# Kernel tuning notes

Hardware: AMD Instinct MI355X
Metric: run time of the kernel (lower is better)

Reference implementation:

```python
import jax, jax.numpy as jnp
import numpy as np

B, T, C, HEAD = 8, 4096, 64, 64

def setup_inputs() -> dict:
    key = jax.random.key(0)
    kx, kk, kq, kv = jax.random.split(key, 4)
    x = jax.random.normal(kx, (B, T, C), dtype=jnp.float32)
    # nn.Linear(n_embd, head_size, bias=False) weight has shape (head_size, n_embd)
    s = 1.0 / np.sqrt(C)
    Wk = jax.random.uniform(kk, (HEAD, C), dtype=jnp.float32, minval=-s, maxval=s)
    Wq = jax.random.uniform(kq, (HEAD, C), dtype=jnp.float32, minval=-s, maxval=s)
    Wv = jax.random.uniform(kv, (HEAD, C), dtype=jnp.float32, minval=-s, maxval=s)
    return {"x": x, "Wk": Wk, "Wq": Wq, "Wv": Wv}

def reference(x, Wk, Wq, Wv):
    Bq, Tq, Cq = x.shape
    k = jnp.einsum('btc,hc->bth', x, Wk)   # (B,T,head)
    q = jnp.einsum('btc,hc->bth', x, Wq)
    v = jnp.einsum('btc,hc->bth', x, Wv)
    scale = Cq ** (-0.5)                    # note: scales by input dim C, as in source
    wei = jnp.einsum('bth,bsh->bts', q, k) * scale  # (B,T,T)
    causal = jnp.tril(jnp.ones((Tq, Tq), dtype=bool))
    wei = jnp.where(causal, wei, -jnp.inf)
    wei = jax.nn.softmax(wei, axis=-1)      # dropout p=0.0 -> no-op
    out = jnp.einsum('bts,bsh->bth', wei, v)
    return out
```

## Files before the change

kernel.cpp:

```cpp
#include <hip/hip_runtime.h>
#include <hip/hip_bf16.h>
#include <math.h>

#define BB 8
#define TT 4096
#define HD 64

typedef __attribute__((ext_vector_type(8))) short short8;
typedef __attribute__((ext_vector_type(4))) float f32x4;
typedef __attribute__((ext_vector_type(16))) float f32x16;
typedef __attribute__((ext_vector_type(2))) unsigned int uint2v;
typedef __attribute__((ext_vector_type(4))) unsigned int uint4v;

#define LOG2E 1.44269504088896f

__device__ __forceinline__ unsigned pack_bf2(float a, float b) {
    unsigned r;
    asm("v_cvt_pk_bf16_f32 %0, %1, %2" : "=v"(r) : "v"(a), "v"(b));
    return r;
}
__device__ __forceinline__ unsigned short bfbits(float f) {
    unsigned r;
    asm("v_cvt_pk_bf16_f32 %0, %1, %2" : "=v"(r) : "v"(f), "v"(f));
    return (unsigned short)r;
}
__device__ __forceinline__ float bf2f(unsigned short u) {
    unsigned v = (unsigned)u << 16;
    return __builtin_bit_cast(float, v);
}
__device__ __forceinline__ float fexp2(float x) {
    return __builtin_amdgcn_exp2f(x);
}
__device__ __forceinline__ short8 cvt8(float4 a, float4 b, float sc) {
    uint4v u;
    u[0] = pack_bf2(a.x * sc, a.y * sc);
    u[1] = pack_bf2(a.z * sc, a.w * sc);
    u[2] = pack_bf2(b.x * sc, b.y * sc);
    u[3] = pack_bf2(b.z * sc, b.w * sc);
    return __builtin_bit_cast(short8, u);
}

__global__ __launch_bounds__(256) void qkv_proj_mfma(
    const float* __restrict__ x,
    const float* __restrict__ Wk, const float* __restrict__ Wq, const float* __restrict__ Wv,
    unsigned short* __restrict__ qo, unsigned short* __restrict__ ko,
    unsigned short* __restrict__ vto)
{
    __shared__ short lds[20480];
    short* xls = lds;
    short* wls = lds + 8192;

    const int tid = threadIdx.x;
    const int l = tid & 63, w = tid >> 6;
    const int hi = l >> 5, c31 = l & 31;
    const long t0 = (long)blockIdx.x * 128;
    const int b = (int)(t0 >> 12);
    const int tl0 = (int)(t0 & 4095);

#pragma unroll
    for (int i = 0; i < 4; ++i) {
        int slot = tid + 256 * i;
        int row = slot >> 3, bl = slot & 7;
        const float* xp = x + (t0 + row) * 64 + 8 * bl;
        float4 a = *(const float4*)xp;
        float4 bq = *(const float4*)(xp + 4);
        *(short8*)&xls[row * 64 + 8 * (bl ^ (row & 7))] = cvt8(a, bq, 1.f);
    }
#pragma unroll
    for (int i = 0; i < 6; ++i) {
        int slot = tid + 256 * i;
        int row = slot >> 3, bl = slot & 7;
        const float* wp;
        float sc;
        if (row < 64)       { wp = Wq + row * 64;         sc = 0.125f * LOG2E; }
        else if (row < 128) { wp = Wk + (row - 64) * 64;  sc = 1.f; }
        else                { wp = Wv + (row - 128) * 64; sc = 1.f; }
        wp += 8 * bl;
        float4 a = *(const float4*)wp;
        float4 bq = *(const float4*)(wp + 4);
        *(short8*)&wls[row * 64 + 8 * (bl ^ (row & 7))] = cvt8(a, bq, sc);
    }
    __syncthreads();

    short8 xf[4];
#pragma unroll
    for (int ki = 0; ki < 4; ++ki) {
        int row = 32 * w + c31;
        xf[ki] = *(const short8*)&xls[row * 64 + 8 * ((2 * ki + hi) ^ (row & 7))];
    }
    f32x16 cqk[4] = {};
#pragma unroll
    for (int nt = 0; nt < 4; ++nt) {
#pragma unroll
        for (int ki = 0; ki < 4; ++ki) {
            int row = 32 * nt + c31;
            short8 wf = *(const short8*)&wls[row * 64 + 8 * ((2 * ki + hi) ^ (row & 7))];
            cqk[nt] = __builtin_amdgcn_mfma_f32_32x32x16_bf16(xf[ki], wf, cqk[nt], 0, 0, 0);
        }
    }
    f32x16 cv[2] = {};
#pragma unroll
    for (int rt = 0; rt < 2; ++rt) {
#pragma unroll
        for (int ki = 0; ki < 4; ++ki) {
            int row = 128 + 32 * rt + c31;
            short8 wf = *(const short8*)&wls[row * 64 + 8 * ((2 * ki + hi) ^ (row & 7))];
            cv[rt] = __builtin_amdgcn_mfma_f32_32x32x16_bf16(wf, xf[ki], cv[rt], 0, 0, 0);
        }
    }
#pragma unroll
    for (int rt = 0; rt < 2; ++rt) {
#pragma unroll
        for (int r = 0; r < 16; ++r) {
            int h = 32 * rt + (r & 3) + 8 * (r >> 2) + 4 * hi;
            vto[((long)b * 64 + h) * 4096 + tl0 + 32 * w + c31] = bfbits(cv[rt][r]);
        }
    }

    __syncthreads();
    short* cb = lds;
#pragma unroll
    for (int nt = 0; nt < 4; ++nt) {
#pragma unroll
        for (int r = 0; r < 16; ++r) {
            int trow = 32 * w + (r & 3) + 8 * (r >> 2) + 4 * hi;
            cb[trow * 136 + 32 * nt + c31] = (short)bfbits(cqk[nt][r]);
        }
    }
    __syncthreads();
    {
        int row = tid >> 1, seg = tid & 1;
        const short8* cp = (const short8*)&cb[row * 136 + seg * 64];
        unsigned short* dst = (seg == 0 ? qo : ko) + (t0 + row) * 64;
#pragma unroll
        for (int i = 0; i < 8; ++i) ((short8*)dst)[i] = cp[i];
    }
}

__global__ __launch_bounds__(256, 3) void attn_mfma(
    const unsigned short* __restrict__ qg,
    const unsigned short* __restrict__ kg,
    const unsigned short* __restrict__ vtg,
    unsigned short* __restrict__ Opart,
    float2* __restrict__ ml,
    float* __restrict__ outg)
{
    __shared__ short kls[3][4096];
    __shared__ short vls[3][4096];

    const int tid = threadIdx.x;
    const int l = tid & 63, w = tid >> 6;
    const int q = l & 31, hi = l >> 5;
    const int qs7 = q & 7;

    const int bid = blockIdx.x;
    const int b = bid & 7;
    const int j = bid >> 3;
    int qt = 0, ci = 0;
    {
        int acc = 0;
        for (int qq = 31; qq >= 0; --qq) {
            int nc = (2 * qq + 17) >> 4;
            if (j < acc + nc) { qt = qq; ci = j - acc; break; }
            acc += nc;
        }
    }
    const int nch = (2 * qt + 17) >> 4;
    int ntile = 2 * qt + 2 - 16 * ci;
    if (ntile > 16) ntile = 16;
    const int c0 = ci * 1024;

    const int q0w = qt * 128 + 32 * w;
    const int qr = q0w + q;
    const int lastg = (q0w + 31) >> 6;

    const unsigned short* qb = qg + ((long)b * TT + qr) * HD;
    short8 qf[4];
#pragma unroll
    for (int ki = 0; ki < 4; ++ki) qf[ki] = *(const short8*)(qb + 16 * ki + 8 * hi);

    int ofs[2][4];
#pragma unroll
    for (int a = 0; a < 2; ++a)
#pragma unroll
        for (int i2 = 0; i2 < 4; ++i2)
            ofs[a][i2] = (32 * a + q) * 128 + 16 * ((2 * i2 + hi) ^ qs7);

    f32x16 oacc[2] = {};
    float m = -INFINITY, lsum = 0.f;

    const unsigned short* kbase = kg + (long)b * TT * HD;
    const unsigned short* vbase = vtg + (long)b * HD * TT;

    const int r8 = l >> 3;
    const int blsw = (l & 7) ^ r8;
    const long koff0 = (long)(8 * w + r8) * HD + 8 * blsw;
    const long voff0 = (long)(8 * w + r8) * TT + 8 * blsw;

#define STAGE(buf_, s_) do {                                                            \
    _Pragma("unroll")                                                                   \
    for (int c_ = 0; c_ < 2; ++c_) {                                                    \
        const unsigned short* kp_ = kbase + (long)(s_) * HD + koff0 + (long)c_ * 32 * HD; \
        const unsigned short* vp_ = vbase + (s_) + voff0 + (long)c_ * 32 * TT;          \
        short* kd_ = &kls[buf_][2048 * c_ + 512 * w];                                   \
        short* vd_ = &vls[buf_][2048 * c_ + 512 * w];                                   \
        __builtin_amdgcn_global_load_lds((const __attribute__((address_space(1))) void*)kp_, \
                                         (__attribute__((address_space(3))) void*)kd_, 16, 0, 0); \
        __builtin_amdgcn_global_load_lds((const __attribute__((address_space(1))) void*)vp_, \
                                         (__attribute__((address_space(3))) void*)vd_, 16, 0, 0); \
    }                                                                                   \
} while (0)

    STAGE(0, c0);
    if (ntile > 1) STAGE(1, c0 + 64);

    int cur = 0, nxt2 = 2;
    for (int it = 0; it < ntile; ++it) {
        const int s0 = c0 + (it << 6);
        if (it + 1 < ntile) asm volatile("s_waitcnt vmcnt(4)" ::: "memory");
        else                asm volatile("s_waitcnt vmcnt(0)" ::: "memory");
        __builtin_amdgcn_s_barrier();
        __builtin_amdgcn_sched_barrier(0);
        if (it + 2 < ntile) STAGE(nxt2, s0 + 128);

        if (s0 <= q0w + 31) {
            const int gti = ci * 16 + it;
            const int nkt = (gti == lastg && (w & 1) == 0) ? 1 : 2;
            const short* kb_ = kls[cur];
            const short* vb_ = vls[cur];

            f32x16 sacc[2] = {};
            __builtin_amdgcn_s_setprio(1);
#pragma unroll
            for (int kt = 0; kt < 2; ++kt) {
                if (kt < nkt) {
#pragma unroll
                    for (int ki = 0; ki < 4; ++ki) {
                        short8 kf = *(const short8*)((const char*)kb_ + ofs[kt][ki]);
                        sacc[kt] = __builtin_amdgcn_mfma_f32_32x32x16_bf16(kf, qf[ki], sacc[kt], 0, 0, 0);
                    }
                }
            }
            __builtin_amdgcn_s_setprio(0);

            if (gti == lastg) {
#pragma unroll
                for (int kt = 0; kt < 2; ++kt) {
                    if (kt >= nkt) continue;
#pragma unroll
                    for (int r = 0; r < 16; ++r) {
                        int kkg = s0 + 32 * kt + (r & 3) + 8 * (r >> 2) + 4 * hi;
                        if (kkg > qr) sacc[kt][r] = -INFINITY;
                    }
                }
            }

            float t8[8];
#pragma unroll
            for (int r = 0; r < 8; ++r) {
                float a = fmaxf(sacc[0][r], sacc[0][r + 8]);
                if (nkt == 2) a = fmaxf(a, fmaxf(sacc[1][r], sacc[1][r + 8]));
                t8[r] = a;
            }
            float pmax = fmaxf(fmaxf(fmaxf(t8[0], t8[1]), fmaxf(t8[2], t8[3])),
                               fmaxf(fmaxf(t8[4], t8[5]), fmaxf(t8[6], t8[7])));
            if (__any(pmax > m + 11.0f)) {
                pmax = fmaxf(pmax, __shfl_xor(pmax, 32, 64));
                float mn = fmaxf(m, pmax);
                float fac = fexp2(m - mn);
                lsum *= fac;
                oacc[0] *= fac;
                oacc[1] *= fac;
                m = mn;
            }

            float rsum = 0.f;
            unsigned ulo[8], uhi[8];
#pragma unroll
            for (int kt = 0; kt < 2; ++kt) {
#pragma unroll
                for (int jj = 0; jj < 4; ++jj) {
                    if (kt < nkt) {
                        float p0 = fexp2(sacc[kt][4 * jj + 0] - m);
                        float p1 = fexp2(sacc[kt][4 * jj + 1] - m);
                        float p2 = fexp2(sacc[kt][4 * jj + 2] - m);
                        float p3 = fexp2(sacc[kt][4 * jj + 3] - m);
                        rsum += (p0 + p1) + (p2 + p3);
                        ulo[4 * kt + jj] = pack_bf2(p0, p1);
                        uhi[4 * kt + jj] = pack_bf2(p2, p3);
                    } else {
                        ulo[4 * kt + jj] = 0;
                        uhi[4 * kt + jj] = 0;
                    }
                }
            }
            lsum += rsum;

            const int nks = 2 * nkt;
#pragma unroll
            for (int ks = 0; ks < 4; ++ks) {
                if (ks >= nks) continue;
                uint2v rlo = __builtin_amdgcn_permlane32_swap(ulo[2 * ks], ulo[2 * ks + 1], false, false);
                uint2v rhi = __builtin_amdgcn_permlane32_swap(uhi[2 * ks], uhi[2 * ks + 1], false, false);
                uint4v paw;
                paw[0] = rlo[0]; paw[1] = rhi[0]; paw[2] = rlo[1]; paw[3] = rhi[1];
                short8 pa = __builtin_bit_cast(short8, paw);
                __builtin_amdgcn_s_setprio(1);
#pragma unroll
                for (int dt = 0; dt < 2; ++dt) {
                    short8 vf = *(const short8*)((const char*)vb_ + ofs[dt][ks]);
                    oacc[dt] = __builtin_amdgcn_mfma_f32_32x32x16_bf16(vf, pa, oacc[dt], 0, 0, 0);
                }
                __builtin_amdgcn_s_setprio(0);
            }
        }
        cur = (cur == 2) ? 0 : cur + 1;
        nxt2 = (nxt2 == 2) ? 0 : nxt2 + 1;
    }
#undef STAGE

    lsum += __shfl_xor(lsum, 32, 64);

    const int lr = 32 * w + q;
    if (nch == 1) {
        const float inv = 1.f / lsum;
        float* op = outg + ((long)b * TT + qr) * HD;
#pragma unroll
        for (int dt = 0; dt < 2; ++dt) {
#pragma unroll
            for (int jj = 0; jj < 4; ++jj) {
                f32x4 o4;
                o4[0] = oacc[dt][4 * jj + 0] * inv;
                o4[1] = oacc[dt][4 * jj + 1] * inv;
                o4[2] = oacc[dt][4 * jj + 2] * inv;
                o4[3] = oacc[dt][4 * jj + 3] * inv;
                *(f32x4*)(op + 32 * dt + 8 * jj + 4 * hi) = o4;
            }
        }
    } else {
        const float inv = lsum > 0.f ? 1.f / lsum : 0.f;
        unsigned short* po = Opart + ((long)(b * 80 + j) * 128 + lr) * 64;
#pragma unroll
        for (int dt = 0; dt < 2; ++dt) {
#pragma unroll
            for (int jj = 0; jj < 4; ++jj) {
                uint2v u;
                u[0] = pack_bf2(oacc[dt][4 * jj + 0] * inv, oacc[dt][4 * jj + 1] * inv);
                u[1] = pack_bf2(oacc[dt][4 * jj + 2] * inv, oacc[dt][4 * jj + 3] * inv);
                *(uint2v*)(po + 32 * dt + 8 * jj + 4 * hi) = u;
            }
        }
        ml[(long)(b * 80 + j) * 128 + lr] = make_float2(m, lsum);
    }
}

__global__ __launch_bounds__(256) void combine(
    const unsigned short* __restrict__ Opart,
    const float2* __restrict__ ml,
    float* __restrict__ outg)
{
    const int bid = blockIdx.x;
    const int b = bid & 7, qt = 8 + (bid >> 3);
    const int nc = (2 * qt + 17) >> 4;
    int jb = 0;
    for (int qq = 31; qq > qt; --qq) jb += (2 * qq + 17) >> 4;

    const int tid = threadIdx.x;
    const int row = tid >> 1, dh = (tid & 1) * 32;
    const long base = (long)(b * 80 + jb) * 128 + row;

    float mv[4], lv[4], M = -INFINITY;
#pragma unroll
    for (int c = 0; c < 4; ++c) {
        mv[c] = -INFINITY; lv[c] = 0.f;
        if (c < nc) {
            float2 t = ml[base + (long)c * 128];
            mv[c] = t.x; lv[c] = t.y;
            M = fmaxf(M, mv[c]);
        }
    }
    float L = 0.f, wt[4];
#pragma unroll
    for (int c = 0; c < 4; ++c) {
        wt[c] = (c < nc) ? lv[c] * fexp2(mv[c] - M) : 0.f;
        L += wt[c];
    }
    float acc[32];
#pragma unroll
    for (int i = 0; i < 32; ++i) acc[i] = 0.f;
#pragma unroll
    for (int c = 0; c < 4; ++c) {
        if (c < nc && wt[c] > 0.f) {
            const short8* op = (const short8*)(Opart + (base + (long)c * 128) * 64 + dh);
#pragma unroll
            for (int i = 0; i < 4; ++i) {
                short8 v = op[i];
#pragma unroll
                for (int e = 0; e < 8; ++e)
                    acc[8 * i + e] += wt[c] * bf2f((unsigned short)v[e]);
            }
        }
    }
    const float invL = 1.f / L;
    float* dst = outg + ((long)b * TT + qt * 128 + row) * HD + dh;
#pragma unroll
    for (int i = 0; i < 8; ++i) {
        f32x4 o;
        o[0] = acc[4 * i + 0] * invL; o[1] = acc[4 * i + 1] * invL;
        o[2] = acc[4 * i + 2] * invL; o[3] = acc[4 * i + 3] * invL;
        *(f32x4*)(dst + 4 * i) = o;
    }
}

extern "C" void kernel_launch(void* const* d_in, const int* in_sizes, int n_in,
                              void* d_out, int out_size, void* d_ws, size_t ws_size,
                              hipStream_t stream) {
    const float* x  = (const float*)d_in[0];
    const float* Wk = (const float*)d_in[1];
    const float* Wq = (const float*)d_in[2];
    const float* Wv = (const float*)d_in[3];
    float* out = (float*)d_out;

    const long N = (long)BB * TT * HD;
    unsigned short* q16 = (unsigned short*)d_ws;
    unsigned short* k16 = q16 + N;
    unsigned short* vt16 = k16 + N;
    unsigned short* Opart = (unsigned short*)((char*)d_ws + 12 * 1024 * 1024);
    float2* mlp = (float2*)((char*)d_ws + 23068672);

    qkv_proj_mfma<<<BB * TT / 128, 256, 0, stream>>>(x, Wk, Wq, Wv, q16, k16, vt16);
    attn_mfma<<<8 * 80, 256, 0, stream>>>(q16, k16, vt16, Opart, mlp, out);
    combine<<<8 * 24, 256, 0, stream>>>(Opart, mlp, out);
}
```

Measured before the change: 61.98 us.

## Give each attention wave two 32-row query tiles to reuse K/V LDS fragments

Each attention block now runs 2 waves instead of 4, and each wave handles 64 query rows as two 32-row tiles (A and B). The K and V fragments read from LDS are shared across both tiles, halving LDS reads per MFMA. Staging is reworked for 128 threads and the vmcnt wait changes to match. The trade-off is higher register pressure (double accumulators and softmax state), a launch bound of 2, and fewer waves per block to hide latency.

```diff
diff --git a/kernel.cpp b/kernel.cpp
--- a/kernel.cpp
+++ b/kernel.cpp
@@ -137,7 +137,7 @@
     }
 }
 
-__global__ __launch_bounds__(256, 3) void attn_mfma(
+__global__ __launch_bounds__(128, 2) void attn_mfma(
     const unsigned short* __restrict__ qg,
     const unsigned short* __restrict__ kg,
     const unsigned short* __restrict__ vtg,
@@ -170,14 +170,18 @@
     if (ntile > 16) ntile = 16;
     const int c0 = ci * 1024;
 
-    const int q0w = qt * 128 + 32 * w;
-    const int qr = q0w + q;
-    const int lastg = (q0w + 31) >> 6;
-
-    const unsigned short* qb = qg + ((long)b * TT + qr) * HD;
-    short8 qf[4];
-#pragma unroll
-    for (int ki = 0; ki < 4; ++ki) qf[ki] = *(const short8*)(qb + 16 * ki + 8 * hi);
+    const int q0b = qt * 128;
+    const int rA = q0b + 64 * w + q;
+    const int rB = rA + 32;
+    const int lastg = 2 * qt + w;
+
+    const unsigned short* qbase = qg + (long)b * TT * HD;
+    short8 qfA[4], qfB[4];
+#pragma unroll
+    for (int ki = 0; ki < 4; ++ki) {
+        qfA[ki] = *(const short8*)(qbase + (long)rA * HD + 16 * ki + 8 * hi);
+        qfB[ki] = *(const short8*)(qbase + (long)rB * HD + 16 * ki + 8 * hi);
+    }
 
     int ofs[2][4];
 #pragma unroll
@@ -186,8 +190,9 @@
         for (int i2 = 0; i2 < 4; ++i2)
             ofs[a][i2] = (32 * a + q) * 128 + 16 * ((2 * i2 + hi) ^ qs7);
 
-    f32x16 oacc[2] = {};
-    float m = -INFINITY, lsum = 0.f;
+    f32x16 oA[2] = {}, oB[2] = {};
+    float mA = -INFINITY, lsA = 0.f;
+    float mB = -INFINITY, lsB = 0.f;
 
     const unsigned short* kbase = kg + (long)b * TT * HD;
     const unsigned short* vbase = vtg + (long)b * HD * TT;
@@ -199,11 +204,11 @@
 
 #define STAGE(buf_, s_) do {                                                            \
     _Pragma("unroll")                                                                   \
-    for (int c_ = 0; c_ < 2; ++c_) {                                                    \
-        const unsigned short* kp_ = kbase + (long)(s_) * HD + koff0 + (long)c_ * 32 * HD; \
-        const unsigned short* vp_ = vbase + (s_) + voff0 + (long)c_ * 32 * TT;          \
-        short* kd_ = &kls[buf_][2048 * c_ + 512 * w];                                   \
-        short* vd_ = &vls[buf_][2048 * c_ + 512 * w];                                   \
+    for (int c_ = 0; c_ < 4; ++c_) {                                                    \
+        const unsigned short* kp_ = kbase + (long)((s_) + 16 * c_) * HD + koff0;        \
+        const unsigned short* vp_ = vbase + (long)(16 * c_) * TT + voff0 + (s_);        \
+        short* kd_ = &kls[buf_][1024 * c_ + 512 * w];                                   \
+        short* vd_ = &vls[buf_][1024 * c_ + 512 * w];                                   \
         __builtin_amdgcn_global_load_lds((const __attribute__((address_space(1))) void*)kp_, \
                                          (__attribute__((address_space(3))) void*)kd_, 16, 0, 0); \
         __builtin_amdgcn_global_load_lds((const __attribute__((address_space(1))) void*)vp_, \
@@ -217,101 +222,148 @@
     int cur = 0, nxt2 = 2;
     for (int it = 0; it < ntile; ++it) {
         const int s0 = c0 + (it << 6);
-        if (it + 1 < ntile) asm volatile("s_waitcnt vmcnt(4)" ::: "memory");
+        if (it + 1 < ntile) asm volatile("s_waitcnt vmcnt(8)" ::: "memory");
         else                asm volatile("s_waitcnt vmcnt(0)" ::: "memory");
         __builtin_amdgcn_s_barrier();
         __builtin_amdgcn_sched_barrier(0);
         if (it + 2 < ntile) STAGE(nxt2, s0 + 128);
 
-        if (s0 <= q0w + 31) {
-            const int gti = ci * 16 + it;
-            const int nkt = (gti == lastg && (w & 1) == 0) ? 1 : 2;
+        const int gti = ci * 16 + it;
+        if (gti <= lastg) {
+            const bool dg = (gti == lastg);
+            const int nktA = dg ? 1 : 2;
             const short* kb_ = kls[cur];
             const short* vb_ = vls[cur];
 
-            f32x16 sacc[2] = {};
+            short8 kf[8];
+#pragma unroll
+            for (int a = 0; a < 2; ++a)
+#pragma unroll
+                for (int i2 = 0; i2 < 4; ++i2)
+                    kf[4 * a + i2] = *(const short8*)((const char*)kb_ + ofs[a][i2]);
+
+            f32x16 sA[2] = {}, sB[2] = {};
             __builtin_amdgcn_s_setprio(1);
 #pragma unroll
-            for (int kt = 0; kt < 2; ++kt) {
-                if (kt < nkt) {
-#pragma unroll
-                    for (int ki = 0; ki < 4; ++ki) {
-                        short8 kf = *(const short8*)((const char*)kb_ + ofs[kt][ki]);
-                        sacc[kt] = __builtin_amdgcn_mfma_f32_32x32x16_bf16(kf, qf[ki], sacc[kt], 0, 0, 0);
+            for (int ki = 0; ki < 4; ++ki) {
+                sA[0] = __builtin_amdgcn_mfma_f32_32x32x16_bf16(kf[ki], qfA[ki], sA[0], 0, 0, 0);
+                sB[0] = __builtin_amdgcn_mfma_f32_32x32x16_bf16(kf[ki], qfB[ki], sB[0], 0, 0, 0);
+            }
+#pragma unroll
+            for (int ki = 0; ki < 4; ++ki) {
+                if (nktA == 2)
+                    sA[1] = __builtin_amdgcn_mfma_f32_32x32x16_bf16(kf[4 + ki], qfA[ki], sA[1], 0, 0, 0);
+                sB[1] = __builtin_amdgcn_mfma_f32_32x32x16_bf16(kf[4 + ki], qfB[ki], sB[1], 0, 0, 0);
+            }
+            __builtin_amdgcn_s_setprio(0);
+
+            if (dg) {
+#pragma unroll
+                for (int r = 0; r < 16; ++r) {
+                    int kkg0 = s0 + (r & 3) + 8 * (r >> 2) + 4 * hi;
+                    if (kkg0 > rA) sA[0][r] = -INFINITY;
+                    if (kkg0 + 32 > rB) sB[1][r] = -INFINITY;
+                }
+            }
+
+            {
+                float t8[8];
+#pragma unroll
+                for (int r = 0; r < 8; ++r) {
+                    float a = fmaxf(sA[0][r], sA[0][r + 8]);
+                    if (nktA == 2) a = fmaxf(a, fmaxf(sA[1][r], sA[1][r + 8]));
+                    t8[r] = a;
+                }
+                float pmax = fmaxf(fmaxf(fmaxf(t8[0], t8[1]), fmaxf(t8[2], t8[3])),
+                                   fmaxf(fmaxf(t8[4], t8[5]), fmaxf(t8[6], t8[7])));
+                if (__any(pmax > mA + 11.0f)) {
+                    pmax = fmaxf(pmax, __shfl_xor(pmax, 32, 64));
+                    float mn = fmaxf(mA, pmax);
+                    float fac = fexp2(mA - mn);
+                    lsA *= fac; oA[0] *= fac; oA[1] *= fac; mA = mn;
+                }
+            }
+            {
+                float t8[8];
+#pragma unroll
+                for (int r = 0; r < 8; ++r)
+                    t8[r] = fmaxf(fmaxf(sB[0][r], sB[0][r + 8]), fmaxf(sB[1][r], sB[1][r + 8]));
+                float pmax = fmaxf(fmaxf(fmaxf(t8[0], t8[1]), fmaxf(t8[2], t8[3])),
+                                   fmaxf(fmaxf(t8[4], t8[5]), fmaxf(t8[6], t8[7])));
+                if (__any(pmax > mB + 11.0f)) {
+                    pmax = fmaxf(pmax, __shfl_xor(pmax, 32, 64));
+                    float mn = fmaxf(mB, pmax);
+                    float fac = fexp2(mB - mn);
+                    lsB *= fac; oB[0] *= fac; oB[1] *= fac; mB = mn;
+                }
+            }
+
+            unsigned uloA[8], uhiA[8], uloB[8], uhiB[8];
+            {
+                float rs = 0.f;
+#pragma unroll
+                for (int kt = 0; kt < 2; ++kt) {
+#pragma unroll
+                    for (int jj = 0; jj < 4; ++jj) {
+                        if (kt < nktA) {
+                            float p0 = fexp2(sA[kt][4 * jj + 0] - mA);
+                            float p1 = fexp2(sA[kt][4 * jj + 1] - mA);
+                            float p2 = fexp2(sA[kt][4 * jj + 2] - mA);
+                            float p3 = fexp2(sA[kt][4 * jj + 3] - mA);
+                            rs += (p0 + p1) + (p2 + p3);
+                            uloA[4 * kt + jj] = pack_bf2(p0, p1);
+                            uhiA[4 * kt + jj] = pack_bf2(p2, p3);
+                        } else {
+                            uloA[4 * kt + jj] = 0; uhiA[4 * kt + jj] = 0;
+                        }
                     }
                 }
-            }
-            __builtin_amdgcn_s_setprio(0);
-
-            if (gti == lastg) {
+                lsA += rs;
+            }
+            {
+                float rs = 0.f;
 #pragma unroll
                 for (int kt = 0; kt < 2; ++kt) {
-                    if (kt >= nkt) continue;
-#pragma unroll
-                    for (int r = 0; r < 16; ++r) {
-                        int kkg = s0 + 32 * kt + (r & 3) + 8 * (r >> 2) + 4 * hi;
-                        if (kkg > qr) sacc[kt][r] = -INFINITY;
+#pragma unroll
+                    for (int jj = 0; jj < 4; ++jj) {
+                        float p0 = fexp2(sB[kt][4 * jj + 0] - mB);
+                        float p1 = fexp2(sB[kt][4 * jj + 1] - mB);
+                        float p2 = fexp2(sB[kt][4 * jj + 2] - mB);
+                        float p3 = fexp2(sB[kt][4 * jj + 3] - mB);
+                        rs += (p0 + p1) + (p2 + p3);
+                        uloB[4 * kt + jj] = pack_bf2(p0, p1);
+                        uhiB[4 * kt + jj] = pack_bf2(p2, p3);
                     }
                 }
-            }
-
-            float t8[8];
-#pragma unroll
-            for (int r = 0; r < 8; ++r) {
-                float a = fmaxf(sacc[0][r], sacc[0][r + 8]);
-                if (nkt == 2) a = fmaxf(a, fmaxf(sacc[1][r], sacc[1][r + 8]));
-                t8[r] = a;
-            }
-            float pmax = fmaxf(fmaxf(fmaxf(t8[0], t8[1]), fmaxf(t8[2], t8[3])),
-                               fmaxf(fmaxf(t8[4], t8[5]), fmaxf(t8[6], t8[7])));
-            if (__any(pmax > m + 11.0f)) {
-                pmax = fmaxf(pmax, __shfl_xor(pmax, 32, 64));
-                float mn = fmaxf(m, pmax);
-                float fac = fexp2(m - mn);
-                lsum *= fac;
-                oacc[0] *= fac;
-                oacc[1] *= fac;
-                m = mn;
-            }
-
-            float rsum = 0.f;
-            unsigned ulo[8], uhi[8];
-#pragma unroll
-            for (int kt = 0; kt < 2; ++kt) {
-#pragma unroll
-                for (int jj = 0; jj < 4; ++jj) {
-                    if (kt < nkt) {
-                        float p0 = fexp2(sacc[kt][4 * jj + 0] - m);
-                        float p1 = fexp2(sacc[kt][4 * jj + 1] - m);
-                        float p2 = fexp2(sacc[kt][4 * jj + 2] - m);
-                        float p3 = fexp2(sacc[kt][4 * jj + 3] - m);
-                        rsum += (p0 + p1) + (p2 + p3);
-                        ulo[4 * kt + jj] = pack_bf2(p0, p1);
-                        uhi[4 * kt + jj] = pack_bf2(p2, p3);
-                    } else {
-                        ulo[4 * kt + jj] = 0;
-                        uhi[4 * kt + jj] = 0;
-                    }
-                }
-            }
-            lsum += rsum;
-
-            const int nks = 2 * nkt;
+                lsB += rs;
+            }
+
+            const int nksA = 2 * nktA;
 #pragma unroll
             for (int ks = 0; ks < 4; ++ks) {
-                if (ks >= nks) continue;
-                uint2v rlo = __builtin_amdgcn_permlane32_swap(ulo[2 * ks], ulo[2 * ks + 1], false, false);
-                uint2v rhi = __builtin_amdgcn_permlane32_swap(uhi[2 * ks], uhi[2 * ks + 1], false, false);
-                uint4v paw;
-                paw[0] = rlo[0]; paw[1] = rhi[0]; paw[2] = rlo[1]; paw[3] = rhi[1];
-                short8 pa = __builtin_bit_cast(short8, paw);
-                __builtin_amdgcn_s_setprio(1);
-#pragma unroll
-                for (int dt = 0; dt < 2; ++dt) {
-                    short8 vf = *(const short8*)((const char*)vb_ + ofs[dt][ks]);
-                    oacc[dt] = __builtin_amdgcn_mfma_f32_32x32x16_bf16(vf, pa, oacc[dt], 0, 0, 0);
-                }
-                __builtin_amdgcn_s_setprio(0);
+                short8 vf0 = *(const short8*)((const char*)vb_ + ofs[0][ks]);
+                short8 vf1 = *(const short8*)((const char*)vb_ + ofs[1][ks]);
+                uint2v rloB = __builtin_amdgcn_permlane32_swap(uloB[2 * ks], uloB[2 * ks + 1], false, false);
+                uint2v rhiB = __builtin_amdgcn_permlane32_swap(uhiB[2 * ks], uhiB[2 * ks + 1], false, false);
+                uint4v pwB; pwB[0] = rloB[0]; pwB[1] = rhiB[0]; pwB[2] = rloB[1]; pwB[3] = rhiB[1];
+                short8 paB = __builtin_bit_cast(short8, pwB);
+                if (ks < nksA) {
+                    uint2v rloA = __builtin_amdgcn_permlane32_swap(uloA[2 * ks], uloA[2 * ks + 1], false, false);
+                    uint2v rhiA = __builtin_amdgcn_permlane32_swap(uhiA[2 * ks], uhiA[2 * ks + 1], false, false);
+                    uint4v pwA; pwA[0] = rloA[0]; pwA[1] = rhiA[0]; pwA[2] = rloA[1]; pwA[3] = rhiA[1];
+                    short8 paA = __builtin_bit_cast(short8, pwA);
+                    __builtin_amdgcn_s_setprio(1);
+                    oA[0] = __builtin_amdgcn_mfma_f32_32x32x16_bf16(vf0, paA, oA[0], 0, 0, 0);
+                    oA[1] = __builtin_amdgcn_mfma_f32_32x32x16_bf16(vf1, paA, oA[1], 0, 0, 0);
+                    oB[0] = __builtin_amdgcn_mfma_f32_32x32x16_bf16(vf0, paB, oB[0], 0, 0, 0);
+                    oB[1] = __builtin_amdgcn_mfma_f32_32x32x16_bf16(vf1, paB, oB[1], 0, 0, 0);
+                    __builtin_amdgcn_s_setprio(0);
+                } else {
+                    __builtin_amdgcn_s_setprio(1);
+                    oB[0] = __builtin_amdgcn_mfma_f32_32x32x16_bf16(vf0, paB, oB[0], 0, 0, 0);
+                    oB[1] = __builtin_amdgcn_mfma_f32_32x32x16_bf16(vf1, paB, oB[1], 0, 0, 0);
+                    __builtin_amdgcn_s_setprio(0);
+                }
             }
         }
         cur = (cur == 2) ? 0 : cur + 1;
@@ -319,38 +371,46 @@
     }
 #undef STAGE
 
-    lsum += __shfl_xor(lsum, 32, 64);
-
-    const int lr = 32 * w + q;
+    lsA += __shfl_xor(lsA, 32, 64);
+    lsB += __shfl_xor(lsB, 32, 64);
+
+    const int lrA = 64 * w + q, lrB = lrA + 32;
     if (nch == 1) {
-        const float inv = 1.f / lsum;
-        float* op = outg + ((long)b * TT + qr) * HD;
+        float* op = outg + (long)b * TT * HD;
+        const float invA = 1.f / lsA, invB = 1.f / lsB;
 #pragma unroll
         for (int dt = 0; dt < 2; ++dt) {
 #pragma unroll
             for (int jj = 0; jj < 4; ++jj) {
-                f32x4 o4;
-                o4[0] = oacc[dt][4 * jj + 0] * inv;
-                o4[1] = oacc[dt][4 * jj + 1] * inv;
-                o4[2] = oacc[dt][4 * jj + 2] * inv;
-                o4[3] = oacc[dt][4 * jj + 3] * inv;
-                *(f32x4*)(op + 32 * dt + 8 * jj + 4 * hi) = o4;
+                f32x4 a4, b4;
+                a4[0] = oA[dt][4 * jj + 0] * invA; a4[1] = oA[dt][4 * jj + 1] * invA;
+                a4[2] = oA[dt][4 * jj + 2] * invA; a4[3] = oA[dt][4 * jj + 3] * invA;
+                b4[0] = oB[dt][4 * jj + 0] * invB; b4[1] = oB[dt][4 * jj + 1] * invB;
+                b4[2] = oB[dt][4 * jj + 2] * invB; b4[3] = oB[dt][4 * jj + 3] * invB;
+                *(f32x4*)(op + (long)rA * HD + 32 * dt + 8 * jj + 4 * hi) = a4;
+                *(f32x4*)(op + (long)rB * HD + 32 * dt + 8 * jj + 4 * hi) = b4;
             }
         }
     } else {
-        const float inv = lsum > 0.f ? 1.f / lsum : 0.f;
-        unsigned short* po = Opart + ((long)(b * 80 + j) * 128 + lr) * 64;
+        const float invA = lsA > 0.f ? 1.f / lsA : 0.f;
+        const float invB = lsB > 0.f ? 1.f / lsB : 0.f;
+        unsigned short* poA = Opart + ((long)(b * 80 + j) * 128 + lrA) * 64;
+        unsigned short* poB = Opart + ((long)(b * 80 + j) * 128 + lrB) * 64;
 #pragma unroll
         for (int dt = 0; dt < 2; ++dt) {
 #pragma unroll
             for (int jj = 0; jj < 4; ++jj) {
-                uint2v u;
-                u[0] = pack_bf2(oacc[dt][4 * jj + 0] * inv, oacc[dt][4 * jj + 1] * inv);
-                u[1] = pack_bf2(oacc[dt][4 * jj + 2] * inv, oacc[dt][4 * jj + 3] * inv);
-                *(uint2v*)(po + 32 * dt + 8 * jj + 4 * hi) = u;
-            }
-        }
-        ml[(long)(b * 80 + j) * 128 + lr] = make_float2(m, lsum);
+                uint2v ua, ub;
+                ua[0] = pack_bf2(oA[dt][4 * jj + 0] * invA, oA[dt][4 * jj + 1] * invA);
+                ua[1] = pack_bf2(oA[dt][4 * jj + 2] * invA, oA[dt][4 * jj + 3] * invA);
+                ub[0] = pack_bf2(oB[dt][4 * jj + 0] * invB, oB[dt][4 * jj + 1] * invB);
+                ub[1] = pack_bf2(oB[dt][4 * jj + 2] * invB, oB[dt][4 * jj + 3] * invB);
+                *(uint2v*)(poA + 32 * dt + 8 * jj + 4 * hi) = ua;
+                *(uint2v*)(poB + 32 * dt + 8 * jj + 4 * hi) = ub;
+            }
+        }
+        ml[(long)(b * 80 + j) * 128 + lrA] = make_float2(mA, lsA);
+        ml[(long)(b * 80 + j) * 128 + lrB] = make_float2(mB, lsB);
     }
 }
 
@@ -429,6 +489,6 @@
     float2* mlp = (float2*)((char*)d_ws + 23068672);
 
     qkv_proj_mfma<<<BB * TT / 128, 256, 0, stream>>>(x, Wk, Wq, Wv, q16, k16, vt16);
-    attn_mfma<<<8 * 80, 256, 0, stream>>>(q16, k16, vt16, Opart, mlp, out);
+    attn_mfma<<<8 * 80, 128, 0, stream>>>(q16, k16, vt16, Opart, mlp, out);
     combine<<<8 * 24, 256, 0, stream>>>(Opart, mlp, out);
 }
```

Result: slower. 75.37 us (+21.6%).

## Process key tiles in pairs with double-buffered pairs and coalesce V^T stores

Applied to the files above, without the earlier changes.

The attention loop now handles two 64-key tiles per iteration, computing both score tiles before a single online-softmax max update. It stages loads into four LDS buffers as double-buffered pairs, which halves the number of barriers and rescale checks per key. The projection kernel now stages V^T through LDS and writes it with 16-byte coalesced stores instead of scattered 2-byte stores. In exchange, attention LDS use grows and the occupancy hint drops from 3 to 2 blocks. The loop also assumes ntile is even, which may break if a chunk has an odd tile count.

```diff
diff --git a/kernel.cpp b/kernel.cpp
--- a/kernel.cpp
+++ b/kernel.cpp
@@ -46,7 +46,7 @@
     unsigned short* __restrict__ qo, unsigned short* __restrict__ ko,
     unsigned short* __restrict__ vto)
 {
-    __shared__ short lds[20480];
+    __shared__ short lds[26112];
     short* xls = lds;
     short* wls = lds + 8192;
 
@@ -108,23 +108,24 @@
             cv[rt] = __builtin_amdgcn_mfma_f32_32x32x16_bf16(wf, xf[ki], cv[rt], 0, 0, 0);
         }
     }
-#pragma unroll
-    for (int rt = 0; rt < 2; ++rt) {
-#pragma unroll
-        for (int r = 0; r < 16; ++r) {
-            int h = 32 * rt + (r & 3) + 8 * (r >> 2) + 4 * hi;
-            vto[((long)b * 64 + h) * 4096 + tl0 + 32 * w + c31] = bfbits(cv[rt][r]);
-        }
-    }
 
     __syncthreads();
     short* cb = lds;
+    short* vb = lds + 17408;
 #pragma unroll
     for (int nt = 0; nt < 4; ++nt) {
 #pragma unroll
         for (int r = 0; r < 16; ++r) {
             int trow = 32 * w + (r & 3) + 8 * (r >> 2) + 4 * hi;
             cb[trow * 136 + 32 * nt + c31] = (short)bfbits(cqk[nt][r]);
+        }
+    }
+#pragma unroll
+    for (int rt = 0; rt < 2; ++rt) {
+#pragma unroll
+        for (int r = 0; r < 16; ++r) {
+            int h = 32 * rt + (r & 3) + 8 * (r >> 2) + 4 * hi;
+            vb[h * 136 + 32 * w + c31] = (short)bfbits(cv[rt][r]);
         }
     }
     __syncthreads();
@@ -135,9 +136,16 @@
 #pragma unroll
         for (int i = 0; i < 8; ++i) ((short8*)dst)[i] = cp[i];
     }
-}
-
-__global__ __launch_bounds__(256, 3) void attn_mfma(
+#pragma unroll
+    for (int i = 0; i < 4; ++i) {
+        int slot = tid + 256 * i;
+        int h = slot >> 4, tc = slot & 15;
+        short8 vv = *(const short8*)&vb[h * 136 + 8 * tc];
+        *(short8*)(vto + ((long)b * 64 + h) * 4096 + tl0 + 8 * tc) = vv;
+    }
+}
+
+__global__ __launch_bounds__(256, 2) void attn_mfma(
     const unsigned short* __restrict__ qg,
     const unsigned short* __restrict__ kg,
     const unsigned short* __restrict__ vtg,
@@ -145,8 +153,8 @@
     float2* __restrict__ ml,
     float* __restrict__ outg)
 {
-    __shared__ short kls[3][4096];
-    __shared__ short vls[3][4096];
+    __shared__ short kls[4][4096];
+    __shared__ short vls[4][4096];
 
     const int tid = threadIdx.x;
     const int l = tid & 63, w = tid >> 6;
@@ -211,46 +219,73 @@
     }                                                                                   \
 } while (0)
 
-    STAGE(0, c0);
-    if (ntile > 1) STAGE(1, c0 + 64);
-
-    int cur = 0, nxt2 = 2;
-    for (int it = 0; it < ntile; ++it) {
-        const int s0 = c0 + (it << 6);
-        if (it + 1 < ntile) asm volatile("s_waitcnt vmcnt(4)" ::: "memory");
+    STAGE(0, c0); STAGE(1, c0 + 64);
+    if (ntile > 2) { STAGE(2, c0 + 128); STAGE(3, c0 + 192); }
+
+    const int npairs = ntile >> 1;
+    for (int p = 0; p < npairs; ++p) {
+        const int sA = c0 + (p << 7);
+        if (p + 1 < npairs) asm volatile("s_waitcnt vmcnt(8)" ::: "memory");
         else                asm volatile("s_waitcnt vmcnt(0)" ::: "memory");
         __builtin_amdgcn_s_barrier();
         __builtin_amdgcn_sched_barrier(0);
-        if (it + 2 < ntile) STAGE(nxt2, s0 + 128);
-
-        if (s0 <= q0w + 31) {
-            const int gti = ci * 16 + it;
-            const int nkt = (gti == lastg && (w & 1) == 0) ? 1 : 2;
-            const short* kb_ = kls[cur];
-            const short* vb_ = vls[cur];
-
-            f32x16 sacc[2] = {};
+
+        const int bs = (p & 1) << 1;
+        const short* kbA = kls[bs],     *vbA = vls[bs];
+        const short* kbB = kls[bs + 1], *vbB = vls[bs + 1];
+        const int gtiA = ci * 16 + 2 * p, gtiB = gtiA + 1;
+        const bool doA = (sA <= q0w + 31);
+        const bool doB = (sA + 64 <= q0w + 31);
+
+        if (doA) {
+            const int nktA = (gtiA == lastg && (w & 1) == 0) ? 1 : 2;
+            const int nktB = (gtiB == lastg && (w & 1) == 0) ? 1 : 2;
+
+            f32x16 sacA[2] = {}, sacB[2] = {};
             __builtin_amdgcn_s_setprio(1);
 #pragma unroll
             for (int kt = 0; kt < 2; ++kt) {
-                if (kt < nkt) {
+                if (kt < nktA) {
 #pragma unroll
                     for (int ki = 0; ki < 4; ++ki) {
-                        short8 kf = *(const short8*)((const char*)kb_ + ofs[kt][ki]);
-                        sacc[kt] = __builtin_amdgcn_mfma_f32_32x32x16_bf16(kf, qf[ki], sacc[kt], 0, 0, 0);
+                        short8 kf = *(const short8*)((const char*)kbA + ofs[kt][ki]);
+                        sacA[kt] = __builtin_amdgcn_mfma_f32_32x32x16_bf16(kf, qf[ki], sacA[kt], 0, 0, 0);
+                    }
+                }
+            }
+            if (doB) {
+#pragma unroll
+                for (int kt = 0; kt < 2; ++kt) {
+                    if (kt < nktB) {
+#pragma unroll
+                        for (int ki = 0; ki < 4; ++ki) {
+                            short8 kf = *(const short8*)((const char*)kbB + ofs[kt][ki]);
+                            sacB[kt] = __builtin_amdgcn_mfma_f32_32x32x16_bf16(kf, qf[ki], sacB[kt], 0, 0, 0);
+                        }
                     }
                 }
             }
             __builtin_amdgcn_s_setprio(0);
 
-            if (gti == lastg) {
+            if (gtiA == lastg) {
 #pragma unroll
                 for (int kt = 0; kt < 2; ++kt) {
-                    if (kt >= nkt) continue;
+                    if (kt >= nktA) continue;
 #pragma unroll
                     for (int r = 0; r < 16; ++r) {
-                        int kkg = s0 + 32 * kt + (r & 3) + 8 * (r >> 2) + 4 * hi;
-                        if (kkg > qr) sacc[kt][r] = -INFINITY;
+                        int kkg = sA + 32 * kt + (r & 3) + 8 * (r >> 2) + 4 * hi;
+                        if (kkg > qr) sacA[kt][r] = -INFINITY;
+                    }
+                }
+            }
+            if (doB && gtiB == lastg) {
+#pragma unroll
+                for (int kt = 0; kt < 2; ++kt) {
+                    if (kt >= nktB) continue;
+#pragma unroll
+                    for (int r = 0; r < 16; ++r) {
+                        int kkg = sA + 64 + 32 * kt + (r & 3) + 8 * (r >> 2) + 4 * hi;
+                        if (kkg > qr) sacB[kt][r] = -INFINITY;
                     }
                 }
             }
@@ -258,8 +293,12 @@
             float t8[8];
 #pragma unroll
             for (int r = 0; r < 8; ++r) {
-                float a = fmaxf(sacc[0][r], sacc[0][r + 8]);
-                if (nkt == 2) a = fmaxf(a, fmaxf(sacc[1][r], sacc[1][r + 8]));
+                float a = fmaxf(sacA[0][r], sacA[0][r + 8]);
+                if (nktA == 2) a = fmaxf(a, fmaxf(sacA[1][r], sacA[1][r + 8]));
+                if (doB) {
+                    a = fmaxf(a, fmaxf(sacB[0][r], sacB[0][r + 8]));
+                    if (nktB == 2) a = fmaxf(a, fmaxf(sacB[1][r], sacB[1][r + 8]));
+                }
                 t8[r] = a;
             }
             float pmax = fmaxf(fmaxf(fmaxf(t8[0], t8[1]), fmaxf(t8[2], t8[3])),
@@ -274,48 +313,88 @@
                 m = mn;
             }
 
-            float rsum = 0.f;
-            unsigned ulo[8], uhi[8];
-#pragma unroll
-            for (int kt = 0; kt < 2; ++kt) {
-#pragma unroll
-                for (int jj = 0; jj < 4; ++jj) {
-                    if (kt < nkt) {
-                        float p0 = fexp2(sacc[kt][4 * jj + 0] - m);
-                        float p1 = fexp2(sacc[kt][4 * jj + 1] - m);
-                        float p2 = fexp2(sacc[kt][4 * jj + 2] - m);
-                        float p3 = fexp2(sacc[kt][4 * jj + 3] - m);
-                        rsum += (p0 + p1) + (p2 + p3);
-                        ulo[4 * kt + jj] = pack_bf2(p0, p1);
-                        uhi[4 * kt + jj] = pack_bf2(p2, p3);
-                    } else {
-                        ulo[4 * kt + jj] = 0;
-                        uhi[4 * kt + jj] = 0;
-                    }
-                }
-            }
-            lsum += rsum;
-
-            const int nks = 2 * nkt;
-#pragma unroll
-            for (int ks = 0; ks < 4; ++ks) {
-                if (ks >= nks) continue;
-                uint2v rlo = __builtin_amdgcn_permlane32_swap(ulo[2 * ks], ulo[2 * ks + 1], false, false);
-                uint2v rhi = __builtin_amdgcn_permlane32_swap(uhi[2 * ks], uhi[2 * ks + 1], false, false);
-                uint4v paw;
-                paw[0] = rlo[0]; paw[1] = rhi[0]; paw[2] = rlo[1]; paw[3] = rhi[1];
-                short8 pa = __builtin_bit_cast(short8, paw);
-                __builtin_amdgcn_s_setprio(1);
-#pragma unroll
-                for (int dt = 0; dt < 2; ++dt) {
-                    short8 vf = *(const short8*)((const char*)vb_ + ofs[dt][ks]);
-                    oacc[dt] = __builtin_amdgcn_mfma_f32_32x32x16_bf16(vf, pa, oacc[dt], 0, 0, 0);
-                }
-                __builtin_amdgcn_s_setprio(0);
-            }
-        }
-        cur = (cur == 2) ? 0 : cur + 1;
-        nxt2 = (nxt2 == 2) ? 0 : nxt2 + 1;
+            {
+                float rs = 0.f;
+                unsigned ulo[8], uhi[8];
+#pragma unroll
+                for (int kt = 0; kt < 2; ++kt) {
+#pragma unroll
+                    for (int jj = 0; jj < 4; ++jj) {
+                        if (kt < nktA) {
+                            float p0 = fexp2(sacA[kt][4 * jj + 0] - m);
+                            float p1 = fexp2(sacA[kt][4 * jj + 1] - m);
+                            float p2 = fexp2(sacA[kt][4 * jj + 2] - m);
+                            float p3 = fexp2(sacA[kt][4 * jj + 3] - m);
+                            rs += (p0 + p1) + (p2 + p3);
+                            ulo[4 * kt + jj] = pack_bf2(p0, p1);
+                            uhi[4 * kt + jj] = pack_bf2(p2, p3);
+                        } else {
+                            ulo[4 * kt + jj] = 0; uhi[4 * kt + jj] = 0;
+                        }
+                    }
+                }
+                lsum += rs;
+                const int nks = 2 * nktA;
+#pragma unroll
+                for (int ks = 0; ks < 4; ++ks) {
+                    if (ks >= nks) continue;
+                    uint2v rlo = __builtin_amdgcn_permlane32_swap(ulo[2 * ks], ulo[2 * ks + 1], false, false);
+                    uint2v rhi = __builtin_amdgcn_permlane32_swap(uhi[2 * ks], uhi[2 * ks + 1], false, false);
+                    uint4v paw;
+                    paw[0] = rlo[0]; paw[1] = rhi[0]; paw[2] = rlo[1]; paw[3] = rhi[1];
+                    short8 pa = __builtin_bit_cast(short8, paw);
+                    __builtin_amdgcn_s_setprio(1);
+#pragma unroll
+                    for (int dt = 0; dt < 2; ++dt) {
+                        short8 vf = *(const short8*)((const char*)vbA + ofs[dt][ks]);
+                        oacc[dt] = __builtin_amdgcn_mfma_f32_32x32x16_bf16(vf, pa, oacc[dt], 0, 0, 0);
+                    }
+                    __builtin_amdgcn_s_setprio(0);
+                }
+            }
+            if (doB) {
+                float rs = 0.f;
+                unsigned ulo[8], uhi[8];
+#pragma unroll
+                for (int kt = 0; kt < 2; ++kt) {
+#pragma unroll
+                    for (int jj = 0; jj < 4; ++jj) {
+                        if (kt < nktB) {
+                            float p0 = fexp2(sacB[kt][4 * jj + 0] - m);
+                            float p1 = fexp2(sacB[kt][4 * jj + 1] - m);
+                            float p2 = fexp2(sacB[kt][4 * jj + 2] - m);
+                            float p3 = fexp2(sacB[kt][4 * jj + 3] - m);
+                            rs += (p0 + p1) + (p2 + p3);
+                            ulo[4 * kt + jj] = pack_bf2(p0, p1);
+                            uhi[4 * kt + jj] = pack_bf2(p2, p3);
+                        } else {
+                            ulo[4 * kt + jj] = 0; uhi[4 * kt + jj] = 0;
+                        }
+                    }
+                }
+                lsum += rs;
+                const int nks = 2 * nktB;
+#pragma unroll
+                for (int ks = 0; ks < 4; ++ks) {
+                    if (ks >= nks) continue;
+                    uint2v rlo = __builtin_amdgcn_permlane32_swap(ulo[2 * ks], ulo[2 * ks + 1], false, false);
+                    uint2v rhi = __builtin_amdgcn_permlane32_swap(uhi[2 * ks], uhi[2 * ks + 1], false, false);
+                    uint4v paw;
+                    paw[0] = rlo[0]; paw[1] = rhi[0]; paw[2] = rlo[1]; paw[3] = rhi[1];
+                    short8 pa = __builtin_bit_cast(short8, paw);
+                    __builtin_amdgcn_s_setprio(1);
+#pragma unroll
+                    for (int dt = 0; dt < 2; ++dt) {
+                        short8 vf = *(const short8*)((const char*)vbB + ofs[dt][ks]);
+                        oacc[dt] = __builtin_amdgcn_mfma_f32_32x32x16_bf16(vf, pa, oacc[dt], 0, 0, 0);
+                    }
+                    __builtin_amdgcn_s_setprio(0);
+                }
+            }
+        }
+
+        __builtin_amdgcn_s_barrier();
+        if (p + 2 < npairs) { STAGE(bs, sA + 256); STAGE(bs + 1, sA + 320); }
     }
 #undef STAGE
 
```

Measured after the change: 70.03 us. 13.0% more time.

## Use finer key-chunk split for attention and stage V-transpose stores through LDS

Applied to the files above, without the earlier changes.

The attention split-K chunk size becomes a runtime parameter. When the workspace is large enough, chunks drop from 16 to 8 key tiles, giving 144 blocks per batch instead of 80 to improve load balance and fill the GPU. The combine kernel is generalised to merge up to 8 partials. Separately, the projection kernel now writes the transposed V through LDS so global stores become coalesced 16-byte writes instead of scattered 2-byte stores. This costs more LDS in the projection kernel and more partial-result traffic in combine.

```diff
diff --git a/kernel.cpp b/kernel.cpp
--- a/kernel.cpp
+++ b/kernel.cpp
@@ -46,7 +46,7 @@
     unsigned short* __restrict__ qo, unsigned short* __restrict__ ko,
     unsigned short* __restrict__ vto)
 {
-    __shared__ short lds[20480];
+    __shared__ short lds[26112];
     short* xls = lds;
     short* wls = lds + 8192;
 
@@ -108,23 +108,24 @@
             cv[rt] = __builtin_amdgcn_mfma_f32_32x32x16_bf16(wf, xf[ki], cv[rt], 0, 0, 0);
         }
     }
-#pragma unroll
-    for (int rt = 0; rt < 2; ++rt) {
-#pragma unroll
-        for (int r = 0; r < 16; ++r) {
-            int h = 32 * rt + (r & 3) + 8 * (r >> 2) + 4 * hi;
-            vto[((long)b * 64 + h) * 4096 + tl0 + 32 * w + c31] = bfbits(cv[rt][r]);
-        }
-    }
 
     __syncthreads();
     short* cb = lds;
+    short* vb = lds + 17408;
 #pragma unroll
     for (int nt = 0; nt < 4; ++nt) {
 #pragma unroll
         for (int r = 0; r < 16; ++r) {
             int trow = 32 * w + (r & 3) + 8 * (r >> 2) + 4 * hi;
             cb[trow * 136 + 32 * nt + c31] = (short)bfbits(cqk[nt][r]);
+        }
+    }
+#pragma unroll
+    for (int rt = 0; rt < 2; ++rt) {
+#pragma unroll
+        for (int r = 0; r < 16; ++r) {
+            int h = 32 * rt + (r & 3) + 8 * (r >> 2) + 4 * hi;
+            vb[h * 136 + 32 * w + c31] = (short)bfbits(cv[rt][r]);
         }
     }
     __syncthreads();
@@ -134,6 +135,13 @@
         unsigned short* dst = (seg == 0 ? qo : ko) + (t0 + row) * 64;
 #pragma unroll
         for (int i = 0; i < 8; ++i) ((short8*)dst)[i] = cp[i];
+    }
+#pragma unroll
+    for (int i = 0; i < 4; ++i) {
+        int slot = tid + 256 * i;
+        int h = slot >> 4, tc = slot & 15;
+        short8 vv = *(const short8*)&vb[h * 136 + 8 * tc];
+        *(short8*)(vto + ((long)b * 64 + h) * 4096 + tl0 + 8 * tc) = vv;
     }
 }
 
@@ -143,11 +151,13 @@
     const unsigned short* __restrict__ vtg,
     unsigned short* __restrict__ Opart,
     float2* __restrict__ ml,
-    float* __restrict__ outg)
+    float* __restrict__ outg,
+    int sh, int CPB)
 {
     __shared__ short kls[3][4096];
     __shared__ short vls[3][4096];
 
+    const int CT = 1 << sh;
     const int tid = threadIdx.x;
     const int l = tid & 63, w = tid >> 6;
     const int q = l & 31, hi = l >> 5;
@@ -160,15 +170,15 @@
     {
         int acc = 0;
         for (int qq = 31; qq >= 0; --qq) {
-            int nc = (2 * qq + 17) >> 4;
+            int nc = (2 * qq + 1 + CT) >> sh;
             if (j < acc + nc) { qt = qq; ci = j - acc; break; }
             acc += nc;
         }
     }
-    const int nch = (2 * qt + 17) >> 4;
-    int ntile = 2 * qt + 2 - 16 * ci;
-    if (ntile > 16) ntile = 16;
-    const int c0 = ci * 1024;
+    const int nch = (2 * qt + 1 + CT) >> sh;
+    int ntile = 2 * qt + 2 - CT * ci;
+    if (ntile > CT) ntile = CT;
+    const int c0 = (ci * CT) << 6;
 
     const int q0w = qt * 128 + 32 * w;
     const int qr = q0w + q;
@@ -224,7 +234,7 @@
         if (it + 2 < ntile) STAGE(nxt2, s0 + 128);
 
         if (s0 <= q0w + 31) {
-            const int gti = ci * 16 + it;
+            const int gti = ci * CT + it;
             const int nkt = (gti == lastg && (w & 1) == 0) ? 1 : 2;
             const short* kb_ = kls[cur];
             const short* vb_ = vls[cur];
@@ -339,7 +349,7 @@
         }
     } else {
         const float inv = lsum > 0.f ? 1.f / lsum : 0.f;
-        unsigned short* po = Opart + ((long)(b * 80 + j) * 128 + lr) * 64;
+        unsigned short* po = Opart + ((long)(b * CPB + j) * 128 + lr) * 64;
 #pragma unroll
         for (int dt = 0; dt < 2; ++dt) {
 #pragma unroll
@@ -350,28 +360,30 @@
                 *(uint2v*)(po + 32 * dt + 8 * jj + 4 * hi) = u;
             }
         }
-        ml[(long)(b * 80 + j) * 128 + lr] = make_float2(m, lsum);
+        ml[(long)(b * CPB + j) * 128 + lr] = make_float2(m, lsum);
     }
 }
 
 __global__ __launch_bounds__(256) void combine(
     const unsigned short* __restrict__ Opart,
     const float2* __restrict__ ml,
-    float* __restrict__ outg)
+    float* __restrict__ outg,
+    int sh, int qtmin, int CPB)
 {
+    const int CT = 1 << sh;
     const int bid = blockIdx.x;
-    const int b = bid & 7, qt = 8 + (bid >> 3);
-    const int nc = (2 * qt + 17) >> 4;
+    const int b = bid & 7, qt = qtmin + (bid >> 3);
+    const int nc = (2 * qt + 1 + CT) >> sh;
     int jb = 0;
-    for (int qq = 31; qq > qt; --qq) jb += (2 * qq + 17) >> 4;
+    for (int qq = 31; qq > qt; --qq) jb += (2 * qq + 1 + CT) >> sh;
 
     const int tid = threadIdx.x;
     const int row = tid >> 1, dh = (tid & 1) * 32;
-    const long base = (long)(b * 80 + jb) * 128 + row;
-
-    float mv[4], lv[4], M = -INFINITY;
-#pragma unroll
-    for (int c = 0; c < 4; ++c) {
+    const long base = (long)(b * CPB + jb) * 128 + row;
+
+    float mv[8], lv[8], M = -INFINITY;
+#pragma unroll
+    for (int c = 0; c < 8; ++c) {
         mv[c] = -INFINITY; lv[c] = 0.f;
         if (c < nc) {
             float2 t = ml[base + (long)c * 128];
@@ -379,9 +391,9 @@
             M = fmaxf(M, mv[c]);
         }
     }
-    float L = 0.f, wt[4];
-#pragma unroll
-    for (int c = 0; c < 4; ++c) {
+    float L = 0.f, wt[8];
+#pragma unroll
+    for (int c = 0; c < 8; ++c) {
         wt[c] = (c < nc) ? lv[c] * fexp2(mv[c] - M) : 0.f;
         L += wt[c];
     }
@@ -389,7 +401,7 @@
 #pragma unroll
     for (int i = 0; i < 32; ++i) acc[i] = 0.f;
 #pragma unroll
-    for (int c = 0; c < 4; ++c) {
+    for (int c = 0; c < 8; ++c) {
         if (c < nc && wt[c] > 0.f) {
             const short8* op = (const short8*)(Opart + (base + (long)c * 128) * 64 + dh);
 #pragma unroll
@@ -425,10 +437,21 @@
     unsigned short* q16 = (unsigned short*)d_ws;
     unsigned short* k16 = q16 + N;
     unsigned short* vt16 = k16 + N;
-    unsigned short* Opart = (unsigned short*)((char*)d_ws + 12 * 1024 * 1024);
-    float2* mlp = (float2*)((char*)d_ws + 23068672);
+    const size_t qkv_bytes = 12582912;
+
+    int sh, CPB;
+    {
+        const size_t need8 = qkv_bytes + (size_t)144 * 8 * 128 * 64 * 2
+                                       + (size_t)144 * 8 * 128 * 8;
+        if (ws_size >= need8) { sh = 3; CPB = 144; }
+        else                  { sh = 4; CPB = 80;  }
+    }
+    const int CT = 1 << sh;
+    unsigned short* Opart = (unsigned short*)((char*)d_ws + qkv_bytes);
+    float2* mlp = (float2*)((char*)d_ws + qkv_bytes + (size_t)CPB * 8 * 128 * 64 * 2);
+    const int qtmin = CT >> 1;
 
     qkv_proj_mfma<<<BB * TT / 128, 256, 0, stream>>>(x, Wk, Wq, Wv, q16, k16, vt16);
-    attn_mfma<<<8 * 80, 256, 0, stream>>>(q16, k16, vt16, Opart, mlp, out);
-    combine<<<8 * 24, 256, 0, stream>>>(Opart, mlp, out);
-}
+    attn_mfma<<<8 * CPB, 256, 0, stream>>>(q16, k16, vt16, Opart, mlp, out, sh, CPB);
+    combine<<<8 * (32 - qtmin), 256, 0, stream>>>(Opart, mlp, out, sh, qtmin, CPB);
+}
```

Result: no change. 61.16 us (-1.3%).
